# Performance work log

Measured on AMD Instinct MI355X. Metric: run time of the kernel, lower is better.

The kernel has to match this reference:

```python
import jax, jax.numpy as jnp
import numpy as np

NF, NA, NC = 100000, 400, 30   # flight, airport, carrier node counts
N = NF + NA + NC               # total nodes after type concatenation
D = 256                        # hidden_channels
B = 3                          # num_bases
R = 4                          # num_relations
E = 250000                     # edges per relation


def setup_inputs() -> dict:
    key = jax.random.key(0)
    ks = jax.random.split(key, 32)
    inp = {
        'x_flight': jax.random.normal(ks[0], (NF, 32), jnp.float32),
        'x_airport': jax.random.normal(ks[1], (NA, 16), jnp.float32),
        'x_carrier': jax.random.normal(ks[2], (NC, 8), jnp.float32),
        # per-type encoders (Linear stored as [in, out])
        'W_f': jax.random.normal(ks[3], (32, D), jnp.float32) * 0.05,
        'b_f': jnp.zeros((D,), jnp.float32),
        'W_a': jax.random.normal(ks[4], (16, D), jnp.float32) * 0.05,
        'b_a': jnp.zeros((D,), jnp.float32),
        'W_c': jax.random.normal(ks[5], (8, D), jnp.float32) * 0.05,
        'b_c': jnp.zeros((D,), jnp.float32),
        # RGCNConv layer 0: basis decomposition W_r = sum_b comp[r,b] * basis[b]
        'basis0': jax.random.normal(ks[6], (B, D, D), jnp.float32) * 0.02,
        'comp0': jax.random.normal(ks[7], (R, B), jnp.float32) * 0.5,
        'root0': jax.random.normal(ks[8], (D, D), jnp.float32) * 0.02,
        'bias0': jnp.zeros((D,), jnp.float32),
        # RGCNConv layer 1
        'basis1': jax.random.normal(ks[9], (B, D, D), jnp.float32) * 0.02,
        'comp1': jax.random.normal(ks[10], (R, B), jnp.float32) * 0.5,
        'root1': jax.random.normal(ks[11], (D, D), jnp.float32) * 0.02,
        'bias1': jnp.zeros((D,), jnp.float32),
        # readout Linear(D -> 1)
        'W_out': jax.random.normal(ks[12], (D, 1), jnp.float32) * 0.05,
        'b_out': jnp.zeros((1,), jnp.float32),
        # per-relation edge lists (local indices within src/dst node type)
        'src0': jax.random.randint(ks[13], (E,), 0, NF),
        'dst0': jax.random.randint(ks[14], (E,), 0, NA),
        'src1': jax.random.randint(ks[15], (E,), 0, NA),
        'dst1': jax.random.randint(ks[16], (E,), 0, NF),
        'src2': jax.random.randint(ks[17], (E,), 0, NF),
        'dst2': jax.random.randint(ks[18], (E,), 0, NC),
        'src3': jax.random.randint(ks[19], (E,), 0, NC),
        'dst3': jax.random.randint(ks[20], (E,), 0, NF),
    }
    return inp


def _rgcn_conv(x, basis, comp, root, bias, edges):
    """PyG RGCNConv with basis decomposition, mean aggregation per relation."""
    W = jnp.einsum('rb,bio->rio', comp, basis)  # [R, D, D]
    out = x @ root + bias                        # root/self transform
    for r, (src, dst) in enumerate(edges):       # R=4 fixed relations
        msg = x[src] @ W[r]                                        # [E, D]
        agg = jax.ops.segment_sum(msg, dst, num_segments=N)        # [N, D]
        deg = jax.ops.segment_sum(jnp.ones((dst.shape[0],), x.dtype), dst,
                                  num_segments=N)
        out = out + agg / jnp.maximum(deg, 1.0)[:, None]           # mean aggr
    return out


def reference(x_flight, x_airport, x_carrier,
              W_f, b_f, W_a, b_a, W_c, b_c,
              basis0, comp0, root0, bias0,
              basis1, comp1, root1, bias1,
              W_out, b_out,
              src0, dst0, src1, dst1, src2, dst2, src3, dst3):
    # per-type encoders + ReLU, then concat into homogeneous node tensor
    hf = jax.nn.relu(x_flight @ W_f + b_f)
    ha = jax.nn.relu(x_airport @ W_a + b_a)
    hc = jax.nn.relu(x_carrier @ W_c + b_c)
    x = jnp.concatenate([hf, ha, hc], axis=0)  # offsets: flight=0, airport=NF, carrier=NF+NA
    edges = [
        (src0, dst0 + NF),        # flight -> airport
        (src1 + NF, dst1),        # airport -> flight
        (src2, dst2 + NF + NA),   # flight -> carrier
        (src3 + NF + NA, dst3),   # carrier -> flight
    ]
    x = jax.nn.relu(_rgcn_conv(x, basis0, comp0, root0, bias0, edges))
    x = jax.nn.relu(_rgcn_conv(x, basis1, comp1, root1, bias1, edges))
    # dropout is identity in eval mode
    return (x[:NF] @ W_out + b_out).squeeze(-1)  # [NF]
```

## Files before the change

### kernel.cpp

```cpp
#include <hip/hip_runtime.h>
#include <hip/hip_bf16.h>
#include <cstdint>
#include <cstddef>

constexpr int NF = 100000;
constexpr int NA = 400;
constexpr int NC = 30;
constexpr int NN = NF + NA + NC;
constexpr int D  = 256;
constexpr int DD = D * D;
constexpr int E  = 250000;
constexpr int NSL = 128;

typedef __attribute__((ext_vector_type(8))) short bf16x8;
typedef __attribute__((ext_vector_type(4))) float f32x4;
typedef __attribute__((ext_vector_type(8))) ushort u16x8;

__device__ inline ushort f2bf(float f) {
    __hip_bfloat16 h = __float2bfloat16(f);
    return __builtin_bit_cast(ushort, h);
}
__device__ inline float bf2f(ushort u) {
    __hip_bfloat16 h = __builtin_bit_cast(__hip_bfloat16, u);
    return __bfloat162float(h);
}

__device__ inline void gload_lds16(const ushort* g, ushort* l) {
    __builtin_amdgcn_global_load_lds(
        (const __attribute__((address_space(1))) void*)g,
        (__attribute__((address_space(3))) void*)l, 16, 0, 0);
}

__global__ __launch_bounds__(256) void encode_all_kernel(
    const float* __restrict__ xf, const float* __restrict__ Wf, const float* __restrict__ bf,
    const float* __restrict__ xa, const float* __restrict__ Wa, const float* __restrict__ ba,
    const float* __restrict__ xc, const float* __restrict__ Wc, const float* __restrict__ bc,
    ushort* __restrict__ hH)
{
    constexpr int FB = NF / 8;
    constexpr int AB = (NA + 7) / 8;
    int c = threadIdx.x;
    int b = blockIdx.x;
    if (b < FB) {
        int base = b * 8;
        float wcol[32];
        #pragma unroll
        for (int k = 0; k < 32; ++k) wcol[k] = Wf[k * D + c];
        float bias = bf[c];
        #pragma unroll
        for (int i = 0; i < 8; ++i) {
            int row = base + i;
            const float* xr = xf + (size_t)row * 32;
            float acc = bias;
            #pragma unroll
            for (int k = 0; k < 32; ++k) acc += xr[k] * wcol[k];
            hH[(size_t)row * D + c] = f2bf(fmaxf(acc, 0.f));
        }
    } else if (b < FB + AB) {
        int base = (b - FB) * 8;
        float wcol[16];
        #pragma unroll
        for (int k = 0; k < 16; ++k) wcol[k] = Wa[k * D + c];
        float bias = ba[c];
        for (int i = 0; i < 8; ++i) {
            int row = base + i;
            if (row >= NA) break;
            const float* xr = xa + (size_t)row * 16;
            float acc = bias;
            #pragma unroll
            for (int k = 0; k < 16; ++k) acc += xr[k] * wcol[k];
            hH[(size_t)(NF + row) * D + c] = f2bf(fmaxf(acc, 0.f));
        }
    } else {
        int base = (b - FB - AB) * 8;
        float wcol[8];
        #pragma unroll
        for (int k = 0; k < 8; ++k) wcol[k] = Wc[k * D + c];
        float bias = bc[c];
        for (int i = 0; i < 8; ++i) {
            int row = base + i;
            if (row >= NC) break;
            const float* xr = xc + (size_t)row * 8;
            float acc = bias;
            #pragma unroll
            for (int k = 0; k < 8; ++k) acc += xr[k] * wcol[k];
            hH[(size_t)(NF + NA + row) * D + c] = f2bf(fmaxf(acc, 0.f));
        }
    }
}

__global__ __launch_bounds__(256) void wsplit_kernel(
    const float* __restrict__ root, ushort* __restrict__ WtH, ushort* __restrict__ WtL)
{
    int n = blockIdx.x, k = threadIdx.x;
    float w = root[(size_t)k * D + n];
    ushort hi = f2bf(w);
    WtH[(size_t)n * D + k] = hi;
    WtL[(size_t)n * D + k] = f2bf(w - bf2f(hi));
}

__global__ __launch_bounds__(256) void wr_kernel(
    const float* __restrict__ basis, const float* __restrict__ comp,
    float* __restrict__ wr)
{
    int idx = blockIdx.x * 256 + threadIdx.x;
    int r = idx >> 16;
    int io = idx & (DD - 1);
    wr[idx] = comp[r * 3 + 0] * basis[io]
            + comp[r * 3 + 1] * basis[DD + io]
            + comp[r * 3 + 2] * basis[2 * DD + io];
}

__global__ __launch_bounds__(256) void deg_count_kernel(
    const int* __restrict__ dst1, const int* __restrict__ dst3,
    int* __restrict__ deg1, int* __restrict__ deg3)
{
    int idx = blockIdx.x * 256 + threadIdx.x;
    if (idx >= 2 * E) return;
    if (idx < E) atomicAdd(&deg1[dst1[idx]], 1);
    else         atomicAdd(&deg3[dst3[idx - E]], 1);
}

__global__ __launch_bounds__(256) void hist02_kernel(
    const int* __restrict__ dst0, const int* __restrict__ dst2,
    int* __restrict__ bh0, int* __restrict__ bh2,
    int* __restrict__ deg13z, float* __restrict__ aggz)
{
    __shared__ int hist[NA];
    int b = blockIdx.x;
    for (int i = b * 256 + threadIdx.x; i < 2 * NF; i += 2 * NSL * 256)
        deg13z[i] = 0;
    for (int i = b * 256 + threadIdx.x; i < (NA + NC) * D; i += 2 * NSL * 256)
        aggz[i] = 0.f;
    bool isR2 = (b >= NSL);
    int sl = isR2 ? b - NSL : b;
    const int* dst = isR2 ? dst2 : dst0;
    int nb = isR2 ? NC : NA;
    for (int i = threadIdx.x; i < nb; i += 256) hist[i] = 0;
    __syncthreads();
    int lo = (int)((long long)E * sl / NSL);
    int hi = (int)((long long)E * (sl + 1) / NSL);
    for (int e = lo + threadIdx.x; e < hi; e += 256)
        atomicAdd(&hist[dst[e]], 1);
    __syncthreads();
    int* bh = isR2 ? (bh2 + sl * NC) : (bh0 + sl * NA);
    for (int i = threadIdx.x; i < nb; i += 256) bh[i] = hist[i];
}

__global__ __launch_bounds__(512) void scan02_kernel(
    int* __restrict__ bh0, int* __restrict__ bh2,
    int* __restrict__ rp0, int* __restrict__ rp2,
    float* __restrict__ inv0, float* __restrict__ inv2)
{
    __shared__ int tot[512];
    __shared__ int exc[512];
    int t = threadIdx.x;
    int cnt = 0;
    if (t < NA) {
        int s = 0;
        for (int sl = 0; sl < NSL; ++sl) {
            int v = bh0[sl * NA + t]; bh0[sl * NA + t] = s; s += v;
        }
        cnt = s;
    } else if (t < NA + NC) {
        int bin = t - NA; int s = 0;
        for (int sl = 0; sl < NSL; ++sl) {
            int v = bh2[sl * NC + bin]; bh2[sl * NC + bin] = s; s += v;
        }
        cnt = s;
    }
    tot[t] = cnt;
    __syncthreads();
    for (int ofs = 1; ofs < 512; ofs <<= 1) {
        int v = (t >= ofs) ? tot[t - ofs] : 0;
        __syncthreads();
        tot[t] += v;
        __syncthreads();
    }
    int ex = tot[t] - cnt;
    if (t < NA) {
        exc[t] = ex;
        rp0[t] = ex;
        inv0[t] = 1.0f / (float)(cnt > 1 ? cnt : 1);
        if (t == 0) { rp0[NA] = E; rp2[NC] = E; }
    } else if (t < NA + NC) {
        exc[t] = ex - E;
        rp2[t - NA] = ex - E;
        inv2[t - NA] = 1.0f / (float)(cnt > 1 ? cnt : 1);
    } else exc[t] = 0;
    __syncthreads();
    for (int idx = t; idx < NSL * NA; idx += 512) {
        int sl = idx / NA; int bin = idx - sl * NA;
        bh0[idx] += exc[bin];
    }
    for (int idx = t; idx < NSL * NC; idx += 512) {
        int sl = idx / NC; int bin = idx - sl * NC;
        bh2[idx] += exc[NA + bin];
    }
}

__global__ __launch_bounds__(256) void fill02_kernel(
    const int* __restrict__ src0, const int* __restrict__ dst0,
    const int* __restrict__ src2, const int* __restrict__ dst2,
    const int* __restrict__ bh0, const int* __restrict__ bh2,
    int* __restrict__ csr0, int* __restrict__ csr2)
{
    __shared__ int cur[NA];
    int b = blockIdx.x;
    bool isR2 = (b >= NSL);
    int sl = isR2 ? b - NSL : b;
    const int* src = isR2 ? src2 : src0;
    const int* dst = isR2 ? dst2 : dst0;
    const int* bh  = isR2 ? (bh2 + sl * NC) : (bh0 + sl * NA);
    int* csr       = isR2 ? csr2 : csr0;
    int nb = isR2 ? NC : NA;
    for (int i = threadIdx.x; i < nb; i += 256) cur[i] = bh[i];
    __syncthreads();
    int lo = (int)((long long)E * sl / NSL);
    int hi = (int)((long long)E * (sl + 1) / NSL);
    for (int e = lo + threadIdx.x; e < hi; e += 256) {
        int pos = atomicAdd(&cur[dst[e]], 1);
        csr[pos] = src[e];
    }
}

__global__ __launch_bounds__(1024) void scanA_kernel(
    const int* __restrict__ deg1, const int* __restrict__ deg3, int* __restrict__ bsum)
{
    __shared__ int s[1024];
    int b = blockIdx.x;
    bool isR3 = (b >= 98);
    const int* deg = isR3 ? deg3 : deg1;
    int chunk = isR3 ? b - 98 : b;
    int i = chunk * 1024 + threadIdx.x;
    int v = (i < NF) ? deg[i] : 0;
    s[threadIdx.x] = v;
    __syncthreads();
    for (int ofs = 512; ofs > 0; ofs >>= 1) {
        if ((int)threadIdx.x < ofs) s[threadIdx.x] += s[threadIdx.x + ofs];
        __syncthreads();
    }
    if (threadIdx.x == 0) bsum[(isR3 ? 128 : 0) + chunk] = s[0];
}

__global__ __launch_bounds__(1024) void scanC_kernel(
    const int* __restrict__ deg1, const int* __restrict__ deg3,
    const int* __restrict__ bsum,
    int* __restrict__ rp1, int* __restrict__ rp3,
    int* __restrict__ cu1, int* __restrict__ cu3,
    float* __restrict__ inv1, float* __restrict__ inv3)
{
    __shared__ int s[1024];
    __shared__ int s2[256];
    int tid = threadIdx.x;
    int b = blockIdx.x;
    int vb = 0;
    if (tid < 256) {
        vb = ((tid & 127) < 98) ? bsum[tid] : 0;
        s2[tid] = vb;
    }
    __syncthreads();
    for (int ofs = 1; ofs < 128; ofs <<= 1) {
        int a = 0;
        if (tid < 256 && (tid & 127) >= ofs) a = s2[tid - ofs];
        __syncthreads();
        if (tid < 256) s2[tid] += a;
        __syncthreads();
    }
    if (tid < 256) s2[tid] -= vb;
    __syncthreads();
    const int* deg; int* rp; int* cu; float* inv; int chunk; int prefix;
    if (b < 98) { deg = deg1; rp = rp1; cu = cu1; inv = inv1; chunk = b;      prefix = s2[chunk]; }
    else        { deg = deg3; rp = rp3; cu = cu3; inv = inv3; chunk = b - 98; prefix = s2[128 + chunk]; }
    int i = chunk * 1024 + tid;
    int v = (i < NF) ? deg[i] : 0;
    s[tid] = v;
    __syncthreads();
    for (int ofs = 1; ofs < 1024; ofs <<= 1) {
        int a = (tid >= ofs) ? s[tid - ofs] : 0;
        __syncthreads();
        s[tid] += a;
        __syncthreads();
    }
    int ex = prefix + s[tid] - v;
    if (i < NF) {
        rp[i] = ex;
        cu[i] = ex;
        inv[i] = 1.0f / (float)(v > 1 ? v : 1);
    }
    if (i == 0) rp[NF] = E;
}

__global__ __launch_bounds__(256) void csr_fill13_kernel(
    const int* __restrict__ src1, const int* __restrict__ dst1,
    const int* __restrict__ src3, const int* __restrict__ dst3,
    int* __restrict__ cu1, int* __restrict__ cu3,
    int* __restrict__ csr1, int* __restrict__ csr3)
{
    int idx = blockIdx.x * 256 + threadIdx.x;
    if (idx >= 2 * E) return;
    if (idx < E) {
        int pos = atomicAdd(&cu1[dst1[idx]], 1);
        csr1[pos] = src1[idx];
    } else {
        int e = idx - E;
        int pos = atomicAdd(&cu3[dst3[e]], 1);
        csr3[pos] = src3[e];
    }
}

__global__ __launch_bounds__(256) void y_kernel(
    const ushort* __restrict__ hH, const float* __restrict__ wr,
    float* __restrict__ y)
{
    int row = blockIdx.x;
    int c = threadIdx.x;
    const ushort* sH = hH + (size_t)(NF + row) * D;
    const float* W = wr + (size_t)((row < NA) ? 1 : 3) * DD;
    float acc = 0.f;
    #pragma unroll 8
    for (int k = 0; k < D; ++k) acc += bf2f(sH[k]) * W[k * D + c];
    y[(size_t)row * D + c] = acc;
}

__global__ __launch_bounds__(512) void gemm_mfma(
    const ushort* __restrict__ A,
    const ushort* __restrict__ WtH, const ushort* __restrict__ WtL,
    const float* __restrict__ bias,
    ushort* __restrict__ G, int nrows)
{
    constexpr int BM = 128, BK = 32;
    constexpr int PLANE = BM * BK;
    constexpr int BUF = 3 * PLANE;
    constexpr int LDW = 36;
    __shared__ __align__(16) ushort lds[3 * BUF];
    const int t = threadIdx.x;
    const int row0 = blockIdx.x * BM;
    const int col0 = blockIdx.y * BM;
    const int w = t >> 6, lane = t & 63;
    const int wm = w >> 2, wn = w & 3;
    const int lr = lane & 15;
    const int lk = lane >> 4;
    f32x4 acc[4][2] = {};

    const ushort* sp[3];
    int dofs[3];
    #pragma unroll
    for (int i = 0; i < 3; ++i) {
        int idx = w * 3 + i;
        int plane = idx >> 3, g = idx & 7;
        const ushort* base = (plane == 0) ? A : (plane == 1) ? WtH : WtL;
        int r = ((plane == 0) ? row0 : col0) + g * 16 + lr;
        if (plane == 0 && r >= nrows) r = nrows - 1;
        sp[i] = base + (size_t)r * D + lk * 8;
        dofs[i] = plane * PLANE + g * 512;
    }

    auto stage = [&](int kt, int buf) {
        ushort* bb = lds + buf * BUF;
        int k0 = kt * BK;
        #pragma unroll
        for (int i = 0; i < 3; ++i)
            gload_lds16(sp[i] + k0, bb + dofs[i]);
    };
    auto compute = [&](int buf) {
        const ushort* base = lds + buf * BUF;
        const ushort* As  = base;
        const ushort* WsH = base + PLANE;
        const ushort* WsL = base + 2 * PLANE;
        bf16x8 bh[2], bl[2];
        #pragma unroll
        for (int ni = 0; ni < 2; ++ni) {
            int off = (wn * 2 + ni) * 512 + lane * 8;
            bh[ni] = *(const bf16x8*)(&WsH[off]);
            bl[ni] = *(const bf16x8*)(&WsL[off]);
        }
        #pragma unroll
        for (int mi = 0; mi < 4; ++mi) {
            int off = (wm * 4 + mi) * 512 + lane * 8;
            bf16x8 ah = *(const bf16x8*)(&As[off]);
            #pragma unroll
            for (int ni = 0; ni < 2; ++ni) {
                acc[mi][ni] = __builtin_amdgcn_mfma_f32_16x16x32_bf16(ah, bh[ni], acc[mi][ni], 0, 0, 0);
                acc[mi][ni] = __builtin_amdgcn_mfma_f32_16x16x32_bf16(ah, bl[ni], acc[mi][ni], 0, 0, 0);
            }
        }
    };

    stage(0, 0);
    stage(1, 1);
    stage(2, 2);
#define PIPE_ITER(KT, PEND)                                        \
    asm volatile("s_waitcnt vmcnt(" #PEND ")" ::: "memory");       \
    __builtin_amdgcn_s_barrier();                                  \
    __builtin_amdgcn_sched_barrier(0);                             \
    compute((KT) % 3);                                             \
    __builtin_amdgcn_s_barrier();                                  \
    __builtin_amdgcn_sched_barrier(0);                             \
    if ((KT) + 3 < 8) stage((KT) + 3, (KT) % 3);
    PIPE_ITER(0, 6)
    PIPE_ITER(1, 6)
    PIPE_ITER(2, 6)
    PIPE_ITER(3, 6)
    PIPE_ITER(4, 6)
    PIPE_ITER(5, 6)
    PIPE_ITER(6, 3)
    PIPE_ITER(7, 0)
#undef PIPE_ITER

    __syncthreads();
    float* S = (float*)lds + (size_t)w * 16 * LDW;
    const int rrow = lane >> 2;
    const int grp  = lane & 3;
    #pragma unroll
    for (int mi = 0; mi < 4; ++mi) {
        __syncthreads();
        #pragma unroll
        for (int ni = 0; ni < 2; ++ni)
            #pragma unroll
            for (int reg = 0; reg < 4; ++reg)
                S[(lk * 4 + reg) * LDW + ni * 16 + lr] = acc[mi][ni][reg];
        __syncthreads();
        int gr = row0 + wm * 64 + mi * 16 + rrow;
        int gc = col0 + wn * 32 + grp * 8;
        if (gr >= nrows) continue;
        float4 f0 = *(const float4*)(&S[rrow * LDW + grp * 8]);
        float4 f1 = *(const float4*)(&S[rrow * LDW + grp * 8 + 4]);
        float4 b0 = *(const float4*)(bias + gc);
        float4 b1 = *(const float4*)(bias + gc + 4);
        float v[8] = {f0.x + b0.x, f0.y + b0.y, f0.z + b0.z, f0.w + b0.w,
                      f1.x + b1.x, f1.y + b1.y, f1.z + b1.z, f1.w + b1.w};
        u16x8 hh;
        #pragma unroll
        for (int j = 0; j < 8; ++j) hh[j] = f2bf(v[j]);
        *(u16x8*)(G + (size_t)gr * D + gc) = hh;
    }
}

__global__ __launch_bounds__(256) void msg_relu_kernel(
    ushort* __restrict__ G,
    const float* __restrict__ y,
    const int* __restrict__ rp1, const int* __restrict__ csr1, const float* __restrict__ inv1,
    const int* __restrict__ rp3, const int* __restrict__ csr3, const float* __restrict__ inv3)
{
    int wid = (blockIdx.x * 256 + threadIdx.x) >> 6;
    int lane = threadIdx.x & 63;
    int row = wid * 2 + (lane >> 5);
    if (row >= NF) return;
    int c = (lane & 31) * 8;
    size_t o = (size_t)row * D + c;
    u16x8 gh = *(const u16x8*)(G + o);
    float v[8];
    #pragma unroll
    for (int j = 0; j < 8; ++j) v[j] = bf2f(gh[j]);
    float m[8] = {};
    int e0 = rp1[row], e1 = rp1[row + 1];
    for (int e = e0; e < e1; ++e) {
        const float* yr = y + (size_t)csr1[e] * D + c;
        float4 u0 = *(const float4*)yr;
        float4 u1 = *(const float4*)(yr + 4);
        m[0] += u0.x; m[1] += u0.y; m[2] += u0.z; m[3] += u0.w;
        m[4] += u1.x; m[5] += u1.y; m[6] += u1.z; m[7] += u1.w;
    }
    float s1 = inv1[row];
    #pragma unroll
    for (int j = 0; j < 8; ++j) { v[j] += s1 * m[j]; m[j] = 0.f; }
    e0 = rp3[row]; e1 = rp3[row + 1];
    for (int e = e0; e < e1; ++e) {
        const float* yr = y + (size_t)(NA + csr3[e]) * D + c;
        float4 u0 = *(const float4*)yr;
        float4 u1 = *(const float4*)(yr + 4);
        m[0] += u0.x; m[1] += u0.y; m[2] += u0.z; m[3] += u0.w;
        m[4] += u1.x; m[5] += u1.y; m[6] += u1.z; m[7] += u1.w;
    }
    float s3 = inv3[row];
    u16x8 oh;
    #pragma unroll
    for (int j = 0; j < 8; ++j) oh[j] = f2bf(fmaxf(v[j] + s3 * m[j], 0.f));
    *(u16x8*)(G + o) = oh;
}

__global__ __launch_bounds__(256) void msg_readout_kernel(
    const ushort* __restrict__ G,
    const float* __restrict__ y,
    const int* __restrict__ rp1, const int* __restrict__ csr1, const float* __restrict__ inv1,
    const int* __restrict__ rp3, const int* __restrict__ csr3, const float* __restrict__ inv3,
    const float* __restrict__ wout, const float* __restrict__ bout,
    float* __restrict__ out)
{
    int wid = (blockIdx.x * 256 + threadIdx.x) >> 6;
    int lane = threadIdx.x & 63;
    int row = wid * 2 + (lane >> 5);
    if (row >= NF) return;
    int c = (lane & 31) * 8;
    size_t o = (size_t)row * D + c;
    u16x8 gh = *(const u16x8*)(G + o);
    float v[8];
    #pragma unroll
    for (int j = 0; j < 8; ++j) v[j] = bf2f(gh[j]);
    float m[8] = {};
    int e0 = rp1[row], e1 = rp1[row + 1];
    for (int e = e0; e < e1; ++e) {
        const float* yr = y + (size_t)csr1[e] * D + c;
        float4 u0 = *(const float4*)yr;
        float4 u1 = *(const float4*)(yr + 4);
        m[0] += u0.x; m[1] += u0.y; m[2] += u0.z; m[3] += u0.w;
        m[4] += u1.x; m[5] += u1.y; m[6] += u1.z; m[7] += u1.w;
    }
    float s1 = inv1[row];
    #pragma unroll
    for (int j = 0; j < 8; ++j) { v[j] += s1 * m[j]; m[j] = 0.f; }
    e0 = rp3[row]; e1 = rp3[row + 1];
    for (int e = e0; e < e1; ++e) {
        const float* yr = y + (size_t)(NA + csr3[e]) * D + c;
        float4 u0 = *(const float4*)yr;
        float4 u1 = *(const float4*)(yr + 4);
        m[0] += u0.x; m[1] += u0.y; m[2] += u0.z; m[3] += u0.w;
        m[4] += u1.x; m[5] += u1.y; m[6] += u1.z; m[7] += u1.w;
    }
    float s3 = inv3[row];
    float4 w0 = *(const float4*)(wout + c);
    float4 w1 = *(const float4*)(wout + c + 4);
    float wv[8] = {w0.x, w0.y, w0.z, w0.w, w1.x, w1.y, w1.z, w1.w};
    float pr = 0.f;
    #pragma unroll
    for (int j = 0; j < 8; ++j) pr += fmaxf(v[j] + s3 * m[j], 0.f) * wv[j];
    pr += __shfl_xor(pr, 1);
    pr += __shfl_xor(pr, 2);
    pr += __shfl_xor(pr, 4);
    pr += __shfl_xor(pr, 8);
    pr += __shfl_xor(pr, 16);
    if ((lane & 31) == 0) out[row] = pr + bout[0];
}

__global__ __launch_bounds__(256) void agg_small_kernel(
    const ushort* __restrict__ hH,
    const int* __restrict__ rp0, const int* __restrict__ csr0,
    const int* __restrict__ rp2, const int* __restrict__ csr2,
    float* __restrict__ agg)
{
    __shared__ float red[4][256];
    int b = blockIdx.x;
    const int* rp; const int* csr; int dstn, chunk, nch; float* arow;
    if (b < NA * 4) { dstn = b >> 2; chunk = b & 3; nch = 4;  rp = rp0; csr = csr0; arow = agg + (size_t)dstn * D; }
    else { int bb = b - NA * 4; dstn = bb >> 6; chunk = bb & 63; nch = 64; rp = rp2; csr = csr2; arow = agg + (size_t)(NA + dstn) * D; }
    int s = rp[dstn], e = rp[dstn + 1];
    int cnt = e - s;
    int lo = s + (int)((long long)cnt * chunk / nch);
    int hi = s + (int)((long long)cnt * (chunk + 1) / nch);
    int w = threadIdx.x >> 6, lane = threadIdx.x & 63;
    int span = hi - lo;
    int wlo = lo + (int)((long long)span * w / 4);
    int whi = lo + (int)((long long)span * (w + 1) / 4);
    int half = lane >> 5;
    int ch8 = (lane & 31) * 8;
    float acc[8] = {};
    int p = wlo;
    for (; p + 1 < whi; p += 2) {
        int r = csr[p + half];
        u16x8 v = *(const u16x8*)(hH + (size_t)r * D + ch8);
        #pragma unroll
        for (int j = 0; j < 8; ++j) acc[j] += bf2f(v[j]);
    }
    if (p < whi && half == 0) {
        int r = csr[p];
        u16x8 v = *(const u16x8*)(hH + (size_t)r * D + ch8);
        #pragma unroll
        for (int j = 0; j < 8; ++j) acc[j] += bf2f(v[j]);
    }
    #pragma unroll
    for (int j = 0; j < 8; ++j) acc[j] += __shfl_xor(acc[j], 32);
    if (lane < 32) {
        #pragma unroll
        for (int j = 0; j < 8; ++j) red[w][ch8 + j] = acc[j];
    }
    __syncthreads();
    int c = threadIdx.x;
    float total = red[0][c] + red[1][c] + red[2][c] + red[3][c];
    atomicAdd(arow + c, total);
}

__global__ __launch_bounds__(256) void smallT_kernel(
    const float* __restrict__ agg, const float* __restrict__ wr,
    const float* __restrict__ inv0, const float* __restrict__ inv2,
    ushort* __restrict__ G)
{
    int row = blockIdx.x;
    int c = threadIdx.x;
    const float* a = agg + (size_t)row * D;
    const float* W = wr + (size_t)((row < NA) ? 0 : 2) * DD;
    float scale = (row < NA) ? inv0[row] : inv2[row - NA];
    float acc = 0.f;
    #pragma unroll 8
    for (int k = 0; k < D; ++k) acc += a[k] * W[k * D + c];
    size_t o = (size_t)(NF + row) * D + c;
    G[o] = f2bf(fmaxf(bf2f(G[o]) + scale * acc, 0.f));
}

extern "C" void kernel_launch(void* const* d_in, const int* in_sizes, int n_in,
                              void* d_out, int out_size, void* d_ws, size_t ws_size,
                              hipStream_t stream)
{
    const float* xf = (const float*)d_in[0];
    const float* xa = (const float*)d_in[1];
    const float* xc = (const float*)d_in[2];
    const float* Wf = (const float*)d_in[3];
    const float* bf = (const float*)d_in[4];
    const float* Wa = (const float*)d_in[5];
    const float* ba = (const float*)d_in[6];
    const float* Wc = (const float*)d_in[7];
    const float* bc = (const float*)d_in[8];
    const float* basis0 = (const float*)d_in[9];
    const float* comp0  = (const float*)d_in[10];
    const float* root0  = (const float*)d_in[11];
    const float* bias0  = (const float*)d_in[12];
    const float* basis1 = (const float*)d_in[13];
    const float* comp1  = (const float*)d_in[14];
    const float* root1  = (const float*)d_in[15];
    const float* bias1  = (const float*)d_in[16];
    const float* Wout = (const float*)d_in[17];
    const float* bout = (const float*)d_in[18];
    const int* src0 = (const int*)d_in[19];
    const int* dst0 = (const int*)d_in[20];
    const int* src1 = (const int*)d_in[21];
    const int* dst1 = (const int*)d_in[22];
    const int* src2 = (const int*)d_in[23];
    const int* dst2 = (const int*)d_in[24];
    const int* src3 = (const int*)d_in[25];
    const int* dst3 = (const int*)d_in[26];
    float* out = (float*)d_out;

    char* ws = (char*)d_ws;
    size_t off = 0;
    auto alloc = [&](size_t bytes) -> char* {
        char* p = ws + off;
        off = (off + bytes + 255) & ~(size_t)255;
        return p;
    };
    ushort* hH  = (ushort*)alloc((size_t)NN * D * 2);
    ushort* gH  = (ushort*)alloc((size_t)NN * D * 2);
    ushort* g2H = hH;
    ushort* WtH = (ushort*)alloc((size_t)DD * 2);
    ushort* WtL = (ushort*)alloc((size_t)DD * 2);
    float* wrbuf  = (float*)alloc((size_t)4 * DD * 4);
    float* ybuf   = (float*)alloc((size_t)(NA + NC) * D * 4);
    float* aggbuf = (float*)alloc((size_t)(NA + NC) * D * 4);
    int*   deg13  = (int*)  alloc((size_t)2 * NF * 4);
    int* deg1 = deg13; int* deg3 = deg13 + NF;
    float* inv1 = (float*)alloc((size_t)NF * 4);
    float* inv3 = (float*)alloc((size_t)NF * 4);
    float* inv0 = (float*)alloc((size_t)NA * 4);
    float* inv2 = (float*)alloc((size_t)NC * 4);
    int* rp0 = (int*)alloc((NA + 1) * 4);
    int* rp1 = (int*)alloc((size_t)(NF + 1) * 4);
    int* rp2 = (int*)alloc((NC + 1) * 4);
    int* rp3 = (int*)alloc((size_t)(NF + 1) * 4);
    int* cu1 = (int*)alloc((size_t)(NF + 1) * 4);
    int* cu3 = (int*)alloc((size_t)(NF + 1) * 4);
    int* csr0 = (int*)alloc((size_t)E * 4);
    int* csr1 = (int*)alloc((size_t)E * 4);
    int* csr2 = (int*)alloc((size_t)E * 4);
    int* csr3 = (int*)alloc((size_t)E * 4);
    int* bsum = (int*)alloc(256 * 4);
    int* bh0  = (int*)alloc((size_t)NSL * NA * 4);
    int* bh2  = (int*)alloc((size_t)NSL * NC * 4);
    (void)ws_size; (void)in_sizes; (void)n_in; (void)out_size;

    hist02_kernel<<<2 * NSL, 256, 0, stream>>>(dst0, dst2, bh0, bh2, deg13, aggbuf);
    scan02_kernel<<<1, 512, 0, stream>>>(bh0, bh2, rp0, rp2, inv0, inv2);
    fill02_kernel<<<2 * NSL, 256, 0, stream>>>(src0, dst0, src2, dst2, bh0, bh2, csr0, csr2);

    deg_count_kernel<<<(2 * E + 255) / 256, 256, 0, stream>>>(dst1, dst3, deg1, deg3);
    scanA_kernel<<<196, 1024, 0, stream>>>(deg1, deg3, bsum);
    scanC_kernel<<<196, 1024, 0, stream>>>(deg1, deg3, bsum, rp1, rp3, cu1, cu3, inv1, inv3);
    csr_fill13_kernel<<<(2 * E + 255) / 256, 256, 0, stream>>>(
        src1, dst1, src3, dst3, cu1, cu3, csr1, csr3);

    encode_all_kernel<<<NF / 8 + (NA + 7) / 8 + (NC + 7) / 8, 256, 0, stream>>>(
        xf, Wf, bf, xa, Wa, ba, xc, Wc, bc, hH);

    wsplit_kernel<<<D, D, 0, stream>>>(root0, WtH, WtL);
    wr_kernel<<<4 * DD / 256, 256, 0, stream>>>(basis0, comp0, wrbuf);
    y_kernel<<<NA + NC, 256, 0, stream>>>(hH, wrbuf, ybuf);
    gemm_mfma<<<dim3((NN + 127) / 128, 2), 512, 0, stream>>>(
        hH, WtH, WtL, bias0, gH, NN);
    agg_small_kernel<<<NA * 4 + NC * 64, 256, 0, stream>>>(
        hH, rp0, csr0, rp2, csr2, aggbuf);
    smallT_kernel<<<NA + NC, 256, 0, stream>>>(aggbuf, wrbuf, inv0, inv2, gH);
    msg_relu_kernel<<<(NF / 2 * 64 + 255) / 256, 256, 0, stream>>>(
        gH, ybuf, rp1, csr1, inv1, rp3, csr3, inv3);

    wsplit_kernel<<<D, D, 0, stream>>>(root1, WtH, WtL);
    wr_kernel<<<4 * DD / 256, 256, 0, stream>>>(basis1, comp1, wrbuf);
    y_kernel<<<NA + NC, 256, 0, stream>>>(gH, wrbuf, ybuf);
    gemm_mfma<<<dim3((NF + 127) / 128, 2), 512, 0, stream>>>(
        gH, WtH, WtL, bias1, g2H, NF);
    msg_readout_kernel<<<(NF / 2 * 64 + 255) / 256, 256, 0, stream>>>(
        g2H, ybuf, rp1, csr1, inv1, rp3, csr3, inv3, Wout, bout, out);
}
```

Measured before the change: 393.6 us.

## Run flight encoder on MFMA with split-bf16 weights and fused airport/carrier path

Replaces the scalar FMA flight encoder (32->256 per node) with an MFMA tile kernel. Each 128-row block loads x as bf16 and the transposed weight as hi/lo bf16 planes into LDS, then stages results through LDS for vectorized bias+ReLU stores. The weight split and transpose is folded into the existing hist02 kernel. Airport and carrier encoding are merged into one branch. The input x is rounded to bf16 with no lo term, which adds some precision loss compared with the fp32 scalar path.

```diff
diff --git a/kernel.cpp b/kernel.cpp
--- a/kernel.cpp
+++ b/kernel.cpp
@@ -11,6 +11,7 @@
 constexpr int DD = D * D;
 constexpr int E  = 250000;
 constexpr int NSL = 128;
+constexpr int FBLK = (NF + 127) / 128;
 
 typedef __attribute__((ext_vector_type(8))) short bf16x8;
 typedef __attribute__((ext_vector_type(4))) float f32x4;
@@ -31,60 +32,118 @@
         (__attribute__((address_space(3))) void*)l, 16, 0, 0);
 }
 
-__global__ __launch_bounds__(256) void encode_all_kernel(
-    const float* __restrict__ xf, const float* __restrict__ Wf, const float* __restrict__ bf,
+__global__ __launch_bounds__(512) void encode_mfma_kernel(
+    const float* __restrict__ xf,
+    const ushort* __restrict__ WtH8, const ushort* __restrict__ WtL8,
+    const float* __restrict__ bfl,
     const float* __restrict__ xa, const float* __restrict__ Wa, const float* __restrict__ ba,
     const float* __restrict__ xc, const float* __restrict__ Wc, const float* __restrict__ bc,
     ushort* __restrict__ hH)
 {
-    constexpr int FB = NF / 8;
-    constexpr int AB = (NA + 7) / 8;
-    int c = threadIdx.x;
-    int b = blockIdx.x;
-    if (b < FB) {
-        int base = b * 8;
-        float wcol[32];
-        #pragma unroll
-        for (int k = 0; k < 32; ++k) wcol[k] = Wf[k * D + c];
-        float bias = bf[c];
-        #pragma unroll
-        for (int i = 0; i < 8; ++i) {
+    const int t = threadIdx.x;
+    const int b = blockIdx.x;
+    if (b >= FBLK) {
+        int c = t & 255;
+        int i0 = t >> 8;
+        int base = (b - FBLK) * 8;
+        for (int i = i0; i < 8; i += 2) {
             int row = base + i;
-            const float* xr = xf + (size_t)row * 32;
-            float acc = bias;
-            #pragma unroll
-            for (int k = 0; k < 32; ++k) acc += xr[k] * wcol[k];
-            hH[(size_t)row * D + c] = f2bf(fmaxf(acc, 0.f));
-        }
-    } else if (b < FB + AB) {
-        int base = (b - FB) * 8;
-        float wcol[16];
-        #pragma unroll
-        for (int k = 0; k < 16; ++k) wcol[k] = Wa[k * D + c];
-        float bias = ba[c];
-        for (int i = 0; i < 8; ++i) {
-            int row = base + i;
-            if (row >= NA) break;
-            const float* xr = xa + (size_t)row * 16;
-            float acc = bias;
-            #pragma unroll
-            for (int k = 0; k < 16; ++k) acc += xr[k] * wcol[k];
+            if (row >= NA + NC) break;
+            float acc;
+            if (row < NA) {
+                const float* xr = xa + (size_t)row * 16;
+                acc = ba[c];
+                #pragma unroll
+                for (int k = 0; k < 16; ++k) acc += xr[k] * Wa[k * D + c];
+            } else {
+                const float* xr = xc + (size_t)(row - NA) * 8;
+                acc = bc[c];
+                #pragma unroll
+                for (int k = 0; k < 8; ++k) acc += xr[k] * Wc[k * D + c];
+            }
             hH[(size_t)(NF + row) * D + c] = f2bf(fmaxf(acc, 0.f));
         }
-    } else {
-        int base = (b - FB - AB) * 8;
-        float wcol[8];
-        #pragma unroll
-        for (int k = 0; k < 8; ++k) wcol[k] = Wc[k * D + c];
-        float bias = bc[c];
-        for (int i = 0; i < 8; ++i) {
-            int row = base + i;
-            if (row >= NC) break;
-            const float* xr = xc + (size_t)row * 8;
-            float acc = bias;
+        return;
+    }
+    constexpr int AOFF = 0, WHOFF = 4096, WLOFF = 12288;
+    __shared__ __align__(16) ushort lds[20480];
+    const int row0 = b * 128;
+    const int w = t >> 6, lane = t & 63;
+    const int wm = w >> 2, wn = w & 3;
+    const int lr = lane & 15;
+    const int lk = lane >> 4;
+    {
+        int r = t >> 2;
+        int seg = (t & 3) * 8;
+        int gr = row0 + r; if (gr >= NF) gr = NF - 1;
+        const float* xr = xf + (size_t)gr * 32 + seg;
+        float4 a0 = *(const float4*)xr;
+        float4 a1 = *(const float4*)(xr + 4);
+        u16x8 bb;
+        bb[0] = f2bf(a0.x); bb[1] = f2bf(a0.y); bb[2] = f2bf(a0.z); bb[3] = f2bf(a0.w);
+        bb[4] = f2bf(a1.x); bb[5] = f2bf(a1.y); bb[6] = f2bf(a1.z); bb[7] = f2bf(a1.w);
+        int g = r >> 4, rr = r & 15, kg = seg >> 3;
+        *(u16x8*)(lds + AOFF + g * 512 + (rr + 16 * kg) * 8) = bb;
+    }
+    #pragma unroll
+    for (int i = 0; i < 4; ++i) {
+        int u = w * 4 + i;
+        int plane = u >> 4, g = u & 15;
+        const ushort* src = (plane ? WtL8 : WtH8) + ((size_t)(g * 16 + lr)) * 32 + lk * 8;
+        ushort* dst = lds + (plane ? WLOFF : WHOFF) + g * 512;
+        gload_lds16(src, dst);
+    }
+    __syncthreads();
+    f32x4 acc[4][4] = {};
+    bf16x8 bhv[4], blv[4];
+    #pragma unroll
+    for (int ni = 0; ni < 4; ++ni) {
+        int off = (wn * 4 + ni) * 512 + lane * 8;
+        bhv[ni] = *(const bf16x8*)(lds + WHOFF + off);
+        blv[ni] = *(const bf16x8*)(lds + WLOFF + off);
+    }
+    #pragma unroll
+    for (int mi = 0; mi < 4; ++mi) {
+        bf16x8 ah = *(const bf16x8*)(lds + AOFF + (wm * 4 + mi) * 512 + lane * 8);
+        #pragma unroll
+        for (int ni = 0; ni < 4; ++ni) {
+            acc[mi][ni] = __builtin_amdgcn_mfma_f32_16x16x32_bf16(ah, bhv[ni], acc[mi][ni], 0, 0, 0);
+            acc[mi][ni] = __builtin_amdgcn_mfma_f32_16x16x32_bf16(ah, blv[ni], acc[mi][ni], 0, 0, 0);
+        }
+    }
+    constexpr int ELDW = 68;
+    float* S = (float*)lds + (size_t)w * 16 * ELDW;
+    const int rrow = lane >> 3;
+    const int grp  = lane & 7;
+    #pragma unroll
+    for (int mi = 0; mi < 4; ++mi) {
+        __syncthreads();
+        #pragma unroll
+        for (int ni = 0; ni < 4; ++ni)
             #pragma unroll
-            for (int k = 0; k < 8; ++k) acc += xr[k] * wcol[k];
-            hH[(size_t)(NF + NA + row) * D + c] = f2bf(fmaxf(acc, 0.f));
+            for (int reg = 0; reg < 4; ++reg)
+                S[(lk * 4 + reg) * ELDW + ni * 16 + lr] = acc[mi][ni][reg];
+        __syncthreads();
+        #pragma unroll
+        for (int it = 0; it < 2; ++it) {
+            int row_i = rrow + it * 8;
+            int gr = row0 + wm * 64 + mi * 16 + row_i;
+            int gc = wn * 64 + grp * 8;
+            if (gr >= NF) continue;
+            float4 f0 = *(const float4*)(&S[row_i * ELDW + grp * 8]);
+            float4 f1 = *(const float4*)(&S[row_i * ELDW + grp * 8 + 4]);
+            float4 b0 = *(const float4*)(bfl + gc);
+            float4 b1 = *(const float4*)(bfl + gc + 4);
+            u16x8 hh;
+            hh[0] = f2bf(fmaxf(f0.x + b0.x, 0.f));
+            hh[1] = f2bf(fmaxf(f0.y + b0.y, 0.f));
+            hh[2] = f2bf(fmaxf(f0.z + b0.z, 0.f));
+            hh[3] = f2bf(fmaxf(f0.w + b0.w, 0.f));
+            hh[4] = f2bf(fmaxf(f1.x + b1.x, 0.f));
+            hh[5] = f2bf(fmaxf(f1.y + b1.y, 0.f));
+            hh[6] = f2bf(fmaxf(f1.z + b1.z, 0.f));
+            hh[7] = f2bf(fmaxf(f1.w + b1.w, 0.f));
+            *(u16x8*)(hH + (size_t)gr * D + gc) = hh;
         }
     }
 }
@@ -124,7 +183,8 @@
 __global__ __launch_bounds__(256) void hist02_kernel(
     const int* __restrict__ dst0, const int* __restrict__ dst2,
     int* __restrict__ bh0, int* __restrict__ bh2,
-    int* __restrict__ deg13z, float* __restrict__ aggz)
+    int* __restrict__ deg13z, float* __restrict__ aggz,
+    const float* __restrict__ Wf, ushort* __restrict__ WfTH, ushort* __restrict__ WfTL)
 {
     __shared__ int hist[NA];
     int b = blockIdx.x;
@@ -132,6 +192,13 @@
         deg13z[i] = 0;
     for (int i = b * 256 + threadIdx.x; i < (NA + NC) * D; i += 2 * NSL * 256)
         aggz[i] = 0.f;
+    if (b < 32) {
+        int n = threadIdx.x;
+        float wv = Wf[(size_t)b * D + n];
+        ushort hi = f2bf(wv);
+        WfTH[(size_t)n * 32 + b] = hi;
+        WfTL[(size_t)n * 32 + b] = f2bf(wv - bf2f(hi));
+    }
     bool isR2 = (b >= NSL);
     int sl = isR2 ? b - NSL : b;
     const int* dst = isR2 ? dst2 : dst0;
@@ -642,6 +709,8 @@
     ushort* g2H = hH;
     ushort* WtH = (ushort*)alloc((size_t)DD * 2);
     ushort* WtL = (ushort*)alloc((size_t)DD * 2);
+    ushort* WfTH = (ushort*)alloc((size_t)D * 32 * 2);
+    ushort* WfTL = (ushort*)alloc((size_t)D * 32 * 2);
     float* wrbuf  = (float*)alloc((size_t)4 * DD * 4);
     float* ybuf   = (float*)alloc((size_t)(NA + NC) * D * 4);
     float* aggbuf = (float*)alloc((size_t)(NA + NC) * D * 4);
@@ -666,7 +735,8 @@
     int* bh2  = (int*)alloc((size_t)NSL * NC * 4);
     (void)ws_size; (void)in_sizes; (void)n_in; (void)out_size;
 
-    hist02_kernel<<<2 * NSL, 256, 0, stream>>>(dst0, dst2, bh0, bh2, deg13, aggbuf);
+    hist02_kernel<<<2 * NSL, 256, 0, stream>>>(dst0, dst2, bh0, bh2, deg13, aggbuf,
+                                               Wf, WfTH, WfTL);
     scan02_kernel<<<1, 512, 0, stream>>>(bh0, bh2, rp0, rp2, inv0, inv2);
     fill02_kernel<<<2 * NSL, 256, 0, stream>>>(src0, dst0, src2, dst2, bh0, bh2, csr0, csr2);
 
@@ -676,8 +746,8 @@
     csr_fill13_kernel<<<(2 * E + 255) / 256, 256, 0, stream>>>(
         src1, dst1, src3, dst3, cu1, cu3, csr1, csr3);
 
-    encode_all_kernel<<<NF / 8 + (NA + 7) / 8 + (NC + 7) / 8, 256, 0, stream>>>(
-        xf, Wf, bf, xa, Wa, ba, xc, Wc, bc, hH);
+    encode_mfma_kernel<<<FBLK + (NA + NC + 7) / 8, 512, 0, stream>>>(
+        xf, WfTH, WfTL, bf, xa, Wa, ba, xc, Wc, bc, hH);
 
     wsplit_kernel<<<D, D, 0, stream>>>(root0, WtH, WtL);
     wr_kernel<<<4 * DD / 256, 256, 0, stream>>>(basis0, comp0, wrbuf);
```

New measurement: 369.9 us. 1.06x faster.
